# Optimization experiments

Measured on AMD Instinct MI355X. Metric: run time of the kernel, lower is better.

Reference implementation:

```python
import jax, jax.numpy as jnp
import numpy as np

D, H, NL, NR, DFF = 512, 8, 8, 16, 2048
MAX_DIST = 2.0
B, L = 4, 512


def sinusoidal_embedding(pos, dim):
    # interleaved: emb[..., 0::2]=sin, emb[..., 1::2]=cos
    half = dim // 2
    freqs = jnp.exp(-jnp.log(10000.0) * jnp.arange(half, dtype=jnp.float32) / half)
    ang = pos[..., None] * freqs  # (..., half)
    return jnp.stack([jnp.sin(ang), jnp.cos(ang)], axis=-1).reshape(*pos.shape, dim)


def setup_inputs() -> dict:
    key = jax.random.key(0)
    ks = jax.random.split(key, 24)
    s = 0.02
    n = lambda k, shape: jax.random.normal(k, shape, jnp.float32) * s
    return {
        'x_t': jax.random.normal(ks[0], (B, L, 3), jnp.float32),
        't': jax.random.randint(ks[1], (B,), 0, 1000),
        'mask': jnp.ones((B, L), bool),
        'x0_self_cond': jax.random.normal(ks[2], (B, L, 3), jnp.float32),
        'Wi': n(ks[3], (3, D)), 'bi': jnp.zeros((D,)),
        'Wsc': n(ks[4], (3, D)), 'bsc': jnp.zeros((D,)),
        'Wt1': n(ks[5], (D, D)), 'bt1': jnp.zeros((D,)),
        'Wt2': n(ks[6], (D, D)), 'bt2': jnp.zeros((D,)),
        'g1': jnp.ones((NL, D)), 'b1': jnp.zeros((NL, D)),
        'Wqkv': n(ks[7], (NL, D, 3 * D)), 'bqkv': jnp.zeros((NL, 3 * D)),
        'Wo': n(ks[8], (NL, D, D)), 'bo': jnp.zeros((NL, D)),
        'Wb': n(ks[9], (NL, NR, H)), 'bb': jnp.zeros((NL, H)),
        'g2': jnp.ones((NL, D)), 'b2': jnp.zeros((NL, D)),
        'Wf1': n(ks[10], (NL, D, DFF)), 'bf1': jnp.zeros((NL, DFF)),
        'Wf2': n(ks[11], (NL, DFF, D)), 'bf2': jnp.zeros((NL, D)),
        'gf': jnp.ones((D,)), 'bf': jnp.zeros((D,)),
        'Wout': n(ks[12], (D, 3)), 'bout': jnp.zeros((3,)),
    }


def _ln(x, g, b):
    m = x.mean(-1, keepdims=True)
    v = ((x - m) ** 2).mean(-1, keepdims=True)
    return (x - m) / jnp.sqrt(v + 1e-5) * g + b


def reference(x_t, t, mask, x0_self_cond, Wi, bi, Wsc, bsc, Wt1, bt1, Wt2, bt2,
              g1, b1, Wqkv, bqkv, Wo, bo, Wb, bb, g2, b2, Wf1, bf1, Wf2, bf2,
              gf, bf, Wout, bout):
    hd = D // H
    scale = hd ** -0.5
    # embedding: input + self-cond + positional + time
    h = (x_t @ Wi + bi) + (x0_self_cond @ Wsc + bsc)  # (B,L,D)
    pos = sinusoidal_embedding(jnp.arange(L, dtype=jnp.float32), D)  # (L,D)
    temb = sinusoidal_embedding(t.astype(jnp.float32), D)  # (B,D)
    temb = jax.nn.gelu(temb @ Wt1 + bt1, approximate=False) @ Wt2 + bt2
    h = h + pos[None] + temb[:, None]
    # shared pairwise RBF features (coords fixed across layers)
    sq = ((x_t[:, :, None] - x_t[:, None]) ** 2).sum(-1)  # (B,L,L)
    dists = jnp.sqrt(jnp.maximum(sq, 1e-12))
    mu = jnp.linspace(0.0, MAX_DIST, NR)
    sigma = MAX_DIST / NR
    rbf = jnp.exp(-(dists[..., None] - mu) ** 2 / (2.0 * sigma ** 2))  # (B,L,L,NR)
    m2 = mask[:, None, None, :]  # (B,1,1,L) key mask

    def block(h, p):
        g1_, b1_, Wqkv_, bqkv_, Wo_, bo_, Wb_, bb_, g2_, b2_, Wf1_, bf1_, Wf2_, bf2_ = p
        x = _ln(h, g1_, b1_)
        qkv = (x @ Wqkv_ + bqkv_).reshape(B, L, 3, H, hd)
        qkv = jnp.moveaxis(qkv, 3, 1)  # (B,H,L,3,hd)
        q, k, v = qkv[..., 0, :], qkv[..., 1, :], qkv[..., 2, :]
        logits = jnp.einsum('bhld,bhmd->bhlm', q, k) * scale
        geo = jnp.einsum('blmr,rh->bhlm', rbf, Wb_) + bb_[None, :, None, None]
        logits = jnp.where(m2, logits + geo, -1e30)
        w = jax.nn.softmax(logits, axis=-1)
        o = jnp.einsum('bhlm,bhmd->blhd', w, v).reshape(B, L, D)
        h = h + (o @ Wo_ + bo_)
        x2 = _ln(h, g2_, b2_)
        h = h + (jax.nn.gelu(x2 @ Wf1_ + bf1_, approximate=False) @ Wf2_ + bf2_)
        return h, None

    h, _ = jax.lax.scan(block, h, (g1, b1, Wqkv, bqkv, Wo, bo, Wb, bb, g2, b2, Wf1, bf1, Wf2, bf2))
    return _ln(h, gf, bf) @ Wout + bout  # (B,L,3) predicted eps
```

## Files before the change

kernel.cpp:

```cpp
#include <hip/hip_runtime.h>
#include <math.h>

#define D 512
#define H 8
#define HD 64
#define NLAYERS 8
#define NRBF 16
#define DFF 2048
#define BATCH 4
#define LSEQ 512

typedef unsigned short u16;
typedef __bf16 bf16x8 __attribute__((ext_vector_type(8)));
typedef float f32x4 __attribute__((ext_vector_type(4)));
typedef u16 u16x4 __attribute__((ext_vector_type(4)));
typedef u16 u16x8 __attribute__((ext_vector_type(8)));

__device__ __forceinline__ float gelu_exact(float v) {
    return 0.5f * v * (1.0f + erff(v * 0.70710678118654752440f));
}

__device__ __forceinline__ u16 f2bf(float x) {
    unsigned u = __builtin_bit_cast(unsigned, x);
    u = (u + 0x7FFFu + ((u >> 16) & 1u)) >> 16;
    return (u16)u;
}

__device__ __forceinline__ void load_lds16(const void* g, void* l) {
    __builtin_amdgcn_global_load_lds(
        (const __attribute__((address_space(1))) void*)g,
        (__attribute__((address_space(3))) void*)l, 16, 0, 0);
}

__global__ __launch_bounds__(256) void k_tes(const int* __restrict__ t,
                                             float* __restrict__ tes)
{
    int b = blockIdx.x, tid = threadIdx.x;
    float tv = (float)t[b];
    float fr = expf(-9.210340371976184f * (float)tid / 256.0f);
    float ang = tv * fr;
    tes[b * D + 2 * tid]     = sinf(ang);
    tes[b * D + 2 * tid + 1] = cosf(ang);
}

__global__ __launch_bounds__(256) void k_gemv(const float* __restrict__ x,
        const float* __restrict__ W, const float* __restrict__ bia,
        float* __restrict__ out, int do_gelu)
{
    __shared__ float part[4][64];
    int b = blockIdx.y;
    int c = threadIdx.x & 63;
    int kt = threadIdx.x >> 6;
    int col = blockIdx.x * 64 + c;
    const float* xr = x + (size_t)b * D;
    float acc = 0.0f;
    #pragma unroll 4
    for (int k = kt * 128; k < kt * 128 + 128; ++k)
        acc = fmaf(xr[k], W[(size_t)k * D + col], acc);
    part[kt][c] = acc;
    __syncthreads();
    if (kt == 0) {
        float v = part[0][c] + part[1][c] + part[2][c] + part[3][c] + bia[col];
        if (do_gelu) v = gelu_exact(v);
        out[(size_t)b * D + col] = v;
    }
}

__global__ __launch_bounds__(512) void k_embed(const float* __restrict__ x_t,
        const float* __restrict__ xsc,
        const float* __restrict__ Wi, const float* __restrict__ bi,
        const float* __restrict__ Wsc, const float* __restrict__ bsc,
        const float* __restrict__ temb, float* __restrict__ h)
{
    int rowid = blockIdx.x;
    int b = rowid >> 9, l = rowid & 511;
    int d = threadIdx.x;
    const float* pt = x_t + (size_t)rowid * 3;
    const float* ps = xsc + (size_t)rowid * 3;
    float acc = bi[d] + bsc[d] + temb[(size_t)b * D + d];
    acc = fmaf(pt[0], Wi[d], acc);
    acc = fmaf(pt[1], Wi[D + d], acc);
    acc = fmaf(pt[2], Wi[2 * D + d], acc);
    acc = fmaf(ps[0], Wsc[d], acc);
    acc = fmaf(ps[1], Wsc[D + d], acc);
    acc = fmaf(ps[2], Wsc[2 * D + d], acc);
    int i = d >> 1;
    float fr = expf(-9.210340371976184f * (float)i / 256.0f);
    float ang = (float)l * fr;
    acc += (d & 1) ? cosf(ang) : sinf(ang);
    h[(size_t)rowid * D + d] = acc;
}

template<bool BF16OUT>
__global__ __launch_bounds__(256) void k_ln(const float* __restrict__ in,
        void* __restrict__ outp,
        const float* __restrict__ g, const float* __restrict__ bta)
{
    int row = blockIdx.x, tid = threadIdx.x;
    const float* xr = in + (size_t)row * D;
    float v0 = xr[tid], v1 = xr[tid + 256];
    float s = v0 + v1;
    #pragma unroll
    for (int o = 32; o >= 1; o >>= 1) s += __shfl_down(s, o);
    __shared__ float ws4[4];
    __shared__ float mb[2];
    int wid = tid >> 6, lane = tid & 63;
    if (lane == 0) ws4[wid] = s;
    __syncthreads();
    if (tid == 0) mb[0] = (ws4[0] + ws4[1] + ws4[2] + ws4[3]) * (1.0f / 512.0f);
    __syncthreads();
    float m = mb[0];
    float d0 = v0 - m, d1 = v1 - m;
    float q = d0 * d0 + d1 * d1;
    #pragma unroll
    for (int o = 32; o >= 1; o >>= 1) q += __shfl_down(q, o);
    if (lane == 0) ws4[wid] = q;
    __syncthreads();
    if (tid == 0) {
        float var = (ws4[0] + ws4[1] + ws4[2] + ws4[3]) * (1.0f / 512.0f);
        mb[1] = 1.0f / sqrtf(var + 1e-5f);
    }
    __syncthreads();
    float inv = mb[1];
    float o0 = d0 * inv * g[tid] + bta[tid];
    float o1 = d1 * inv * g[tid + 256] + bta[tid + 256];
    if constexpr (BF16OUT) {
        u16* o = (u16*)outp;
        o[(size_t)row * D + tid]       = f2bf(o0);
        o[(size_t)row * D + tid + 256] = f2bf(o1);
    } else {
        float* o = (float*)outp;
        o[(size_t)row * D + tid]       = o0;
        o[(size_t)row * D + tid + 256] = o1;
    }
}

__global__ __launch_bounds__(256) void k_wt(const float* __restrict__ W,
        u16* __restrict__ Wt, int K, int N, size_t wstride)
{
    W  += (size_t)blockIdx.z * K * N;
    Wt += (size_t)blockIdx.z * wstride;
    __shared__ u16 t[32][33];
    int bx = blockIdx.x * 32;
    int by = blockIdx.y * 32;
    int tx = threadIdx.x & 31, ty = threadIdx.x >> 5;
    #pragma unroll
    for (int i = 0; i < 4; ++i)
        t[ty + i * 8][tx] = f2bf(W[(size_t)(by + ty + i * 8) * N + bx + tx]);
    __syncthreads();
    #pragma unroll
    for (int i = 0; i < 4; ++i)
        Wt[(size_t)(bx + ty + i * 8) * K + by + tx] = t[tx][ty + i * 8];
}

template<int MODE, int KSPLIT, int TM, int TN, bool BATCHED>
__global__ __launch_bounds__(256) void k_mfma(const u16* __restrict__ A,
        const u16* __restrict__ Bt, const float* __restrict__ bias,
        float* __restrict__ C, u16* __restrict__ Cb,
        int M, int N, int K, int lda, int ldb, int ldc, float scale,
        size_t ab, size_t ah, size_t bb, size_t bh, size_t cb2, size_t ch)
{
    constexpr int nA = TM / 64;
    constexpr int nB = TN / 64;
    constexpr int WM = (TN == 128) ? 2 : 4;
    constexpr int WN = 4 / WM;
    constexpr int MF = TM / (16 * WM);
    constexpr int NF = TN / (16 * WN);
    __shared__ u16 sA[2][TM * 32];
    __shared__ u16 sB[2][TN * 32];
    int tid = threadIdx.x;
    int bm = blockIdx.y * TM, bn = blockIdx.x * TN;
    int wave = tid >> 6, lane = tid & 63;
    int wm = wave / WN, wn = wave % WN;

    size_t aoff = 0, boff = 0, coff = 0;
    if constexpr (BATCHED) {
        int z = blockIdx.z, zb = z >> 3, zh = z & 7;
        aoff = (size_t)zb * ab + (size_t)zh * ah;
        boff = (size_t)zb * bb + (size_t)zh * bh;
        coff = (size_t)zb * cb2 + (size_t)zh * ch;
    }
    const int Kc = K / KSPLIT;
    const int nt = Kc >> 5;
    const int kb = (KSPLIT > 1 ? (int)blockIdx.z : 0) * Kc;

    const u16* pA[nA]; int idA[nA];
    const u16* pB[nB]; int idB[nB];
    #pragma unroll
    for (int s = 0; s < nA; ++s) {
        int id = tid + s * 256;
        int r = ((id >> 6) << 4) | (id & 15);
        int kg = (id >> 4) & 3;
        idA[s] = id;
        pA[s] = A + aoff + (size_t)(bm + r) * lda + kb + kg * 8;
    }
    #pragma unroll
    for (int s = 0; s < nB; ++s) {
        int id = tid + s * 256;
        int r = ((id >> 6) << 4) | (id & 15);
        int kg = (id >> 4) & 3;
        idB[s] = id;
        pB[s] = Bt + boff + (size_t)(bn + r) * ldb + kb + kg * 8;
    }

    #pragma unroll
    for (int s = 0; s < nA; ++s) { load_lds16(pA[s], &sA[0][idA[s] * 8]); pA[s] += 32; }
    #pragma unroll
    for (int s = 0; s < nB; ++s) { load_lds16(pB[s], &sB[0][idB[s] * 8]); pB[s] += 32; }

    f32x4 acc[MF][NF] = {};
    int cur = 0;
    for (int t = 0; t < nt; ++t) {
        if (t + 1 < nt) {
            int nxt = cur ^ 1;
            #pragma unroll
            for (int s = 0; s < nA; ++s) { load_lds16(pA[s], &sA[nxt][idA[s] * 8]); pA[s] += 32; }
            #pragma unroll
            for (int s = 0; s < nB; ++s) { load_lds16(pB[s], &sB[nxt][idB[s] * 8]); pB[s] += 32; }
            if constexpr (nA + nB == 4)
                asm volatile("s_waitcnt vmcnt(4)" ::: "memory");
            else
                asm volatile("s_waitcnt vmcnt(3)" ::: "memory");
        } else {
            asm volatile("s_waitcnt vmcnt(0)" ::: "memory");
        }
        __builtin_amdgcn_s_barrier();
        asm volatile("" ::: "memory");
        const u16* bufA = sA[cur];
        const u16* bufB = sB[cur];
        bf16x8 af[MF], bg[NF];
        #pragma unroll
        for (int i = 0; i < MF; ++i)
            af[i] = *(const bf16x8*)(bufA + ((wm * MF + i) * 64 + lane) * 8);
        #pragma unroll
        for (int i = 0; i < NF; ++i)
            bg[i] = *(const bf16x8*)(bufB + ((wn * NF + i) * 64 + lane) * 8);
        #pragma unroll
        for (int mi = 0; mi < MF; ++mi)
            #pragma unroll
            for (int ni = 0; ni < NF; ++ni)
                acc[mi][ni] = __builtin_amdgcn_mfma_f32_16x16x32_bf16(
                    af[mi], bg[ni], acc[mi][ni], 0, 0, 0);
        asm volatile("" ::: "memory");
        __builtin_amdgcn_s_barrier();
        cur ^= 1;
    }

    int cr = (lane >> 4) << 2;
    int cc = lane & 15;
    #pragma unroll
    for (int ni = 0; ni < NF; ++ni) {
        int col = bn + (wn * NF + ni) * 16 + cc;
        float bv = 0.0f;
        if (bias && !(KSPLIT > 1 && blockIdx.z != 0)) bv = bias[col];
        #pragma unroll
        for (int mi = 0; mi < MF; ++mi) {
            #pragma unroll
            for (int r = 0; r < 4; ++r) {
                int row = bm + (wm * MF + mi) * 16 + cr + r;
                float v = acc[mi][ni][r] + bv;
                size_t idx = coff + (size_t)row * ldc + col;
                if constexpr (MODE == 1) {
                    Cb[idx] = f2bf(gelu_exact(v));
                } else if constexpr (MODE == 2) {
                    if constexpr (KSPLIT > 1) atomicAdd(&C[idx], v);
                    else C[idx] += v;
                } else if constexpr (MODE == 3) {
                    Cb[idx] = f2bf(v);
                } else {
                    C[idx] = fmaf(v, scale, C[idx]);
                }
            }
        }
    }
}

__global__ __launch_bounds__(512) void k_geo(const float* __restrict__ x_t,
        const float* __restrict__ Wb_l, const float* __restrict__ bb_l,
        float* __restrict__ geo)
{
    __shared__ float wbs[NRBF * H];
    __shared__ float bbs[H];
    int tid = threadIdx.x;
    int b = blockIdx.x >> 9, l = blockIdx.x & 511;
    if (tid < NRBF * H) wbs[tid] = Wb_l[tid];
    if (tid < H) bbs[tid] = bb_l[tid];
    __syncthreads();
    int m = tid;
    const float* pl = x_t + ((size_t)b * LSEQ + l) * 3;
    const float* pm = x_t + ((size_t)b * LSEQ + m) * 3;
    float dx = pl[0] - pm[0], dy = pl[1] - pm[1], dz = pl[2] - pm[2];
    float dist = sqrtf(fmaxf(dx * dx + dy * dy + dz * dz, 1e-12f));
    float e[NRBF];
    #pragma unroll
    for (int r = 0; r < NRBF; ++r) {
        float dd = dist - (2.0f / 15.0f) * (float)r;
        e[r] = expf(-dd * dd * 32.0f);
    }
    #pragma unroll
    for (int hh = 0; hh < H; ++hh) {
        float acc = bbs[hh];
        #pragma unroll
        for (int r = 0; r < NRBF; ++r) acc = fmaf(e[r], wbs[r * H + hh], acc);
        geo[(((size_t)b * H + hh) * LSEQ + l) * LSEQ + m] = acc;
    }
}

__global__ __launch_bounds__(256) void k_vt(const u16* __restrict__ qkv,
                                            u16* __restrict__ vT)
{
    __shared__ u16 s[64 * 65];
    int z = blockIdx.y, b = z >> 3, hh = z & 7;
    int l0 = blockIdx.x * 64;
    const u16* src = qkv + (size_t)(b * LSEQ + l0) * (3 * D) + 2 * D + hh * 64;
    int tid = threadIdx.x;
    int rl = tid >> 3;
    int ch = (tid & 7) * 8;
    #pragma unroll
    for (int it = 0; it < 2; ++it) {
        int l = rl + it * 32;
        u16x8 v = *(const u16x8*)(src + (size_t)l * (3 * D) + ch);
        #pragma unroll
        for (int j = 0; j < 8; ++j) s[l * 65 + ch + j] = v[j];
    }
    __syncthreads();
    u16* dst = vT + (size_t)z * (HD * LSEQ) + l0;
    int lane = tid & 63;
    int h0 = tid >> 6;
    #pragma unroll
    for (int it = 0; it < 16; ++it) {
        int hd = h0 * 16 + it;
        dst[(size_t)hd * LSEQ + lane] = s[lane * 65 + hd];
    }
}

__global__ __launch_bounds__(256) void k_attn(const u16* __restrict__ qkv,
        const u16* __restrict__ vT, const float* __restrict__ geo,
        u16* __restrict__ O)
{
    __shared__ u16 sQ[4096];
    __shared__ u16 sK[2][4096];
    __shared__ u16 sV[2][4096];
    __shared__ float sG[2][4096];
    __shared__ u16 sP[4][1024];
    int tid = threadIdx.x;
    int wave = tid >> 6, lane = tid & 63;
    int qt = blockIdx.x, z = blockIdx.y;
    int b = z >> 3, hh = z & 7;
    int q0 = qt * 64;

    const u16* qbase = qkv + (size_t)b * LSEQ * (3 * D) + hh * 64;
    const u16* vbase = vT + (size_t)z * (HD * LSEQ);
    const float* gbase = geo + ((size_t)z * LSEQ + q0) * LSEQ;

    {
        #pragma unroll
        for (int i = 0; i < 2; ++i) {
            int id = tid + i * 256;
            int f = id >> 7, s = (id >> 6) & 1, ln = id & 63;
            load_lds16(qbase + (size_t)(q0 + f * 16 + (ln & 15)) * (3 * D)
                       + s * 32 + ((ln >> 4) & 3) * 8, sQ + id * 8);
        }
    }
    auto stage = [&](int kt, int buf) {
        #pragma unroll
        for (int i = 0; i < 2; ++i) {
            int id = tid + i * 256;
            int f = id >> 7, s = (id >> 6) & 1, ln = id & 63;
            load_lds16(qbase + (size_t)(kt * 64 + f * 16 + (ln & 15)) * (3 * D)
                       + D + s * 32 + ((ln >> 4) & 3) * 8, sK[buf] + id * 8);
        }
        #pragma unroll
        for (int i = 0; i < 2; ++i) {
            int id = tid + i * 256;
            int f = id >> 7, s = (id >> 6) & 1, ln = id & 63;
            load_lds16(vbase + (size_t)(f * 16 + (ln & 15)) * LSEQ
                       + kt * 64 + s * 32 + ((ln >> 4) & 3) * 8, sV[buf] + id * 8);
        }
        #pragma unroll
        for (int i = 0; i < 4; ++i) {
            int id = tid + i * 256;
            load_lds16(gbase + (size_t)(id >> 4) * LSEQ + kt * 64 + (id & 15) * 4,
                       &sG[buf][id * 4]);
        }
    };
    stage(0, 0);

    f32x4 oacc[4] = {};
    float m_run[4] = {-1e30f, -1e30f, -1e30f, -1e30f};
    float l_run[4] = {0.f, 0.f, 0.f, 0.f};
    bf16x8 aq[2];
    u16* pw = sP[wave];
    int qgrp = lane >> 4;
    int cc = lane & 15;

    int cur = 0;
    for (int kt = 0; kt < 8; ++kt) {
        if (kt + 1 < 8) {
            stage(kt + 1, cur ^ 1);
            asm volatile("s_waitcnt vmcnt(8)" ::: "memory");
        } else {
            asm volatile("s_waitcnt vmcnt(0)" ::: "memory");
        }
        __builtin_amdgcn_s_barrier();
        asm volatile("" ::: "memory");
        if (kt == 0) {
            aq[0] = *(const bf16x8*)(sQ + (wave * 128 + lane) * 8);
            aq[1] = *(const bf16x8*)(sQ + (wave * 128 + 64 + lane) * 8);
        }
        f32x4 sc[4] = {};
        #pragma unroll
        for (int f = 0; f < 4; ++f) {
            #pragma unroll
            for (int s = 0; s < 2; ++s) {
                bf16x8 bk = *(const bf16x8*)(sK[cur] + (f * 128 + s * 64 + lane) * 8);
                sc[f] = __builtin_amdgcn_mfma_f32_16x16x32_bf16(aq[s], bk, sc[f], 0, 0, 0);
            }
        }
        float lg[4][4];
        #pragma unroll
        for (int f = 0; f < 4; ++f)
            #pragma unroll
            for (int r = 0; r < 4; ++r)
                lg[f][r] = fmaf(sc[f][r], 0.125f,
                    sG[cur][(wave * 16 + qgrp * 4 + r) * 64 + f * 16 + cc]);
        float tmax[4];
        #pragma unroll
        for (int r = 0; r < 4; ++r) {
            tmax[r] = fmaxf(fmaxf(lg[0][r], lg[1][r]), fmaxf(lg[2][r], lg[3][r]));
            #pragma unroll
            for (int o = 1; o <= 8; o <<= 1)
                tmax[r] = fmaxf(tmax[r], __shfl_xor(tmax[r], o));
        }
        float corr[4], rs[4];
        #pragma unroll
        for (int r = 0; r < 4; ++r) {
            float mnew = fmaxf(m_run[r], tmax[r]);
            corr[r] = expf(m_run[r] - mnew);
            m_run[r] = mnew;
            rs[r] = 0.f;
        }
        float pf[4][4];
        #pragma unroll
        for (int f = 0; f < 4; ++f)
            #pragma unroll
            for (int r = 0; r < 4; ++r) {
                float p = expf(lg[f][r] - m_run[r]);
                pf[f][r] = p;
                rs[r] += p;
            }
        #pragma unroll
        for (int r = 0; r < 4; ++r) {
            #pragma unroll
            for (int o = 1; o <= 8; o <<= 1)
                rs[r] += __shfl_xor(rs[r], o);
            l_run[r] = l_run[r] * corr[r] + rs[r];
        }
        #pragma unroll
        for (int fd = 0; fd < 4; ++fd)
            #pragma unroll
            for (int r = 0; r < 4; ++r)
                oacc[fd][r] *= corr[r];
        #pragma unroll
        for (int f = 0; f < 4; ++f)
            #pragma unroll
            for (int r = 0; r < 4; ++r) {
                int m = f * 16 + cc;
                int q = qgrp * 4 + r;
                pw[(m >> 5) * 512 + ((m >> 3) & 3) * 128 + q * 8 + (m & 7)]
                    = f2bf(pf[f][r]);
            }
        asm volatile("s_waitcnt lgkmcnt(0)" ::: "memory");
        __builtin_amdgcn_sched_barrier(0);
        bf16x8 ap0 = *(const bf16x8*)(pw + lane * 8);
        bf16x8 ap1 = *(const bf16x8*)(pw + 512 + lane * 8);
        #pragma unroll
        for (int fd = 0; fd < 4; ++fd) {
            #pragma unroll
            for (int s = 0; s < 2; ++s) {
                bf16x8 bv = *(const bf16x8*)(sV[cur] + (fd * 128 + s * 64 + lane) * 8);
                oacc[fd] = __builtin_amdgcn_mfma_f32_16x16x32_bf16(
                    s ? ap1 : ap0, bv, oacc[fd], 0, 0, 0);
            }
        }
        asm volatile("" ::: "memory");
        __builtin_amdgcn_s_barrier();
        cur ^= 1;
    }

    float linv[4];
    #pragma unroll
    for (int r = 0; r < 4; ++r) linv[r] = 1.0f / l_run[r];
    u16* obase = O + ((size_t)(b * LSEQ + q0 + wave * 16)) * D + hh * 64;
    #pragma unroll
    for (int fd = 0; fd < 4; ++fd)
        #pragma unroll
        for (int r = 0; r < 4; ++r)
            obase[(size_t)(qgrp * 4 + r) * D + fd * 16 + cc]
                = f2bf(oacc[fd][r] * linv[r]);
}

__global__ __launch_bounds__(64) void k_out(const float* __restrict__ x,
        const float* __restrict__ Wout, const float* __restrict__ bout,
        float* __restrict__ out)
{
    int row = blockIdx.x, lane = threadIdx.x;
    const float* xr = x + (size_t)row * D;
    float v[8];
    #pragma unroll
    for (int j = 0; j < 8; ++j) v[j] = xr[lane * 8 + j];
    #pragma unroll
    for (int c = 0; c < 3; ++c) {
        float s = 0.0f;
        #pragma unroll
        for (int j = 0; j < 8; ++j)
            s = fmaf(v[j], Wout[(size_t)(lane * 8 + j) * 3 + c], s);
        #pragma unroll
        for (int o = 32; o >= 1; o >>= 1) s += __shfl_xor(s, o);
        if (lane == 0) out[(size_t)row * 3 + c] = s + bout[c];
    }
}

extern "C" void kernel_launch(void* const* d_in, const int* in_sizes, int n_in,
                              void* d_out, int out_size, void* d_ws, size_t ws_size,
                              hipStream_t stream)
{
    const float* x_t  = (const float*)d_in[0];
    const int*   t    = (const int*)d_in[1];
    const float* xsc  = (const float*)d_in[3];
    const float* Wi   = (const float*)d_in[4];
    const float* bi   = (const float*)d_in[5];
    const float* Wsc  = (const float*)d_in[6];
    const float* bsc  = (const float*)d_in[7];
    const float* Wt1  = (const float*)d_in[8];
    const float* bt1  = (const float*)d_in[9];
    const float* Wt2  = (const float*)d_in[10];
    const float* bt2  = (const float*)d_in[11];
    const float* g1   = (const float*)d_in[12];
    const float* b1   = (const float*)d_in[13];
    const float* Wqkv = (const float*)d_in[14];
    const float* bqkv = (const float*)d_in[15];
    const float* Wo   = (const float*)d_in[16];
    const float* bo   = (const float*)d_in[17];
    const float* Wb   = (const float*)d_in[18];
    const float* bbp  = (const float*)d_in[19];
    const float* g2   = (const float*)d_in[20];
    const float* b2   = (const float*)d_in[21];
    const float* Wf1  = (const float*)d_in[22];
    const float* bf1  = (const float*)d_in[23];
    const float* Wf2  = (const float*)d_in[24];
    const float* bf2  = (const float*)d_in[25];
    const float* gf   = (const float*)d_in[26];
    const float* bfv  = (const float*)d_in[27];
    const float* Wout = (const float*)d_in[28];
    const float* bout = (const float*)d_in[29];

    const size_t M1 = 1u << 20;
    float* ws    = (float*)d_ws;
    float* tes   = ws;
    float* temb1 = tes + 2048;
    float* temb  = temb1 + 2048;
    float* h     = temb + 2048;
    float* geo   = h + M1;
    float* x     = geo;
    u16*   qkvb  = (u16*)(geo + 8 * M1);
    u16*   vT    = qkvb + 3 * M1;
    u16*   xb    = vT + M1;
    u16*   obuf  = xb + M1;
    u16*   ffh   = obuf + M1;
    u16*   wbase = ffh + 4 * M1;
    const size_t WQ = 1536 * 512, WO = 512 * 512, WF1 = 512 * 2048,
                 WF2 = 2048 * 512;
    const size_t WL = WQ + WO + WF1 + WF2;
    size_t need8 = (size_t)((char*)(wbase + 8 * WL) - (char*)d_ws);
    bool pre = ws_size >= need8;

    if (pre) {
        k_wt<<<dim3(48, 16, 8), 256, 0, stream>>>(Wqkv, wbase, 512, 1536, WL);
        k_wt<<<dim3(16, 16, 8), 256, 0, stream>>>(Wo, wbase + WQ, 512, 512, WL);
        k_wt<<<dim3(64, 16, 8), 256, 0, stream>>>(Wf1, wbase + WQ + WO, 512, 2048, WL);
        k_wt<<<dim3(16, 64, 8), 256, 0, stream>>>(Wf2, wbase + WQ + WO + WF1, 2048, 512, WL);
    }

    k_tes<<<BATCH, 256, 0, stream>>>(t, tes);
    k_gemv<<<dim3(8, BATCH), 256, 0, stream>>>(tes, Wt1, bt1, temb1, 1);
    k_gemv<<<dim3(8, BATCH), 256, 0, stream>>>(temb1, Wt2, bt2, temb, 0);
    k_embed<<<BATCH * LSEQ, 512, 0, stream>>>(x_t, xsc, Wi, bi, Wsc, bsc, temb, h);

    for (int layer = 0; layer < NLAYERS; ++layer) {
        const float* g1_   = g1 + layer * D;
        const float* b1_   = b1 + layer * D;
        const float* Wqkv_ = Wqkv + (size_t)layer * D * 3 * D;
        const float* bqkv_ = bqkv + (size_t)layer * 3 * D;
        const float* Wo_   = Wo + (size_t)layer * D * D;
        const float* bo_   = bo + (size_t)layer * D;
        const float* Wb_   = Wb + (size_t)layer * NRBF * H;
        const float* bb_   = bbp + (size_t)layer * H;
        const float* g2_   = g2 + layer * D;
        const float* b2_   = b2 + layer * D;
        const float* Wf1_  = Wf1 + (size_t)layer * D * DFF;
        const float* bf1_  = bf1 + (size_t)layer * DFF;
        const float* Wf2_  = Wf2 + (size_t)layer * DFF * D;
        const float* bf2_  = bf2 + (size_t)layer * D;

        u16* wq  = wbase + (pre ? (size_t)layer * WL : 0);
        u16* wo_ = wq + WQ;
        u16* wf1 = wo_ + WO;
        u16* wf2 = wf1 + WF1;
        if (!pre) {
            k_wt<<<dim3(48, 16, 1), 256, 0, stream>>>(Wqkv_, wq, 512, 1536, 0);
            k_wt<<<dim3(16, 16, 1), 256, 0, stream>>>(Wo_, wo_, 512, 512, 0);
            k_wt<<<dim3(64, 16, 1), 256, 0, stream>>>(Wf1_, wf1, 512, 2048, 0);
            k_wt<<<dim3(16, 64, 1), 256, 0, stream>>>(Wf2_, wf2, 2048, 512, 0);
        }

        k_ln<true><<<BATCH * LSEQ, 256, 0, stream>>>(h, xb, g1_, b1_);
        k_mfma<3, 1, 128, 128, false><<<dim3(12, 16, 1), 256, 0, stream>>>(
            xb, wq, bqkv_, nullptr, qkvb, 2048, 1536, 512,
            512, 512, 1536, 0.f, 0, 0, 0, 0, 0, 0);
        k_vt<<<dim3(8, 32), 256, 0, stream>>>(qkvb, vT);
        k_geo<<<BATCH * LSEQ, 512, 0, stream>>>(x_t, Wb_, bb_, geo);
        k_attn<<<dim3(8, 32), 256, 0, stream>>>(qkvb, vT, geo, obuf);
        k_mfma<2, 4, 128, 128, false><<<dim3(4, 16, 4), 256, 0, stream>>>(
            obuf, wo_, bo_, h, nullptr, 2048, 512, 512,
            512, 512, 512, 0.f, 0, 0, 0, 0, 0, 0);
        k_ln<true><<<BATCH * LSEQ, 256, 0, stream>>>(h, xb, g2_, b2_);
        k_mfma<1, 1, 128, 128, false><<<dim3(16, 16, 1), 256, 0, stream>>>(
            xb, wf1, bf1_, nullptr, ffh, 2048, 2048, 512,
            512, 512, 2048, 0.f, 0, 0, 0, 0, 0, 0);
        k_mfma<2, 4, 128, 128, false><<<dim3(4, 16, 4), 256, 0, stream>>>(
            ffh, wf2, bf2_, h, nullptr, 2048, 512, 2048,
            2048, 2048, 512, 0.f, 0, 0, 0, 0, 0, 0);
    }

    k_ln<false><<<BATCH * LSEQ, 256, 0, stream>>>(h, x, gf, bfv);
    k_out<<<BATCH * LSEQ, 64, 0, stream>>>(x, Wout, bout, (float*)d_out);
}
```

Before: 1.318 ms.

## Fuse geometric bias into attention via distance lookup table; fuse V transpose

Each layer no longer materializes the B*H*L*L geometric bias tensor. A per-layer table of the RBF-projected bias is precomputed over distances in [0,4) at 1/1024 resolution, and the attention kernel computes pairwise distances from x_t in LDS and looks up the bias. The QKV GEMM epilogue now writes the V part directly in transposed layout, which removes the separate k_vt kernel. This saves a large global write and read of the bias per layer and two launches per layer. In exchange the bias is a nearest-sample approximation, with distances clamped at the table end where the RBF terms are effectively zero.

```diff
diff --git a/kernel.cpp b/kernel.cpp
--- a/kernel.cpp
+++ b/kernel.cpp
@@ -153,12 +153,34 @@
         Wt[(size_t)(bx + ty + i * 8) * K + by + tx] = t[tx][ty + i * 8];
 }
 
-template<int MODE, int KSPLIT, int TM, int TN, bool BATCHED>
+__global__ __launch_bounds__(256) void k_tab(const float* __restrict__ Wb,
+        const float* __restrict__ bbp, float* __restrict__ tabs)
+{
+    int layer = blockIdx.x;
+    int tid = threadIdx.x;
+    __shared__ float wbs[NRBF * H];
+    __shared__ float bbs[H];
+    if (tid < NRBF * H) wbs[tid] = Wb[layer * NRBF * H + tid];
+    if (tid < H) bbs[tid] = bbp[layer * H + tid];
+    __syncthreads();
+    for (int i = tid; i < H * 4096; i += 256) {
+        int hh = i >> 12, ii = i & 4095;
+        float d = (float)ii * (1.0f / 1024.0f);
+        float acc = bbs[hh];
+        #pragma unroll
+        for (int r = 0; r < NRBF; ++r) {
+            float dd = d - (2.0f / 15.0f) * (float)r;
+            acc = fmaf(expf(-dd * dd * 32.0f), wbs[r * H + hh], acc);
+        }
+        tabs[(size_t)layer * (H * 4096) + i] = acc;
+    }
+}
+
+template<int MODE, int KSPLIT, int TM, int TN>
 __global__ __launch_bounds__(256) void k_mfma(const u16* __restrict__ A,
         const u16* __restrict__ Bt, const float* __restrict__ bias,
-        float* __restrict__ C, u16* __restrict__ Cb,
-        int M, int N, int K, int lda, int ldb, int ldc, float scale,
-        size_t ab, size_t ah, size_t bb, size_t bh, size_t cb2, size_t ch)
+        float* __restrict__ C, u16* __restrict__ Cb, u16* __restrict__ vTp,
+        int M, int N, int K, int lda, int ldb, int ldc)
 {
     constexpr int nA = TM / 64;
     constexpr int nB = TN / 64;
@@ -173,13 +195,6 @@
     int wave = tid >> 6, lane = tid & 63;
     int wm = wave / WN, wn = wave % WN;
 
-    size_t aoff = 0, boff = 0, coff = 0;
-    if constexpr (BATCHED) {
-        int z = blockIdx.z, zb = z >> 3, zh = z & 7;
-        aoff = (size_t)zb * ab + (size_t)zh * ah;
-        boff = (size_t)zb * bb + (size_t)zh * bh;
-        coff = (size_t)zb * cb2 + (size_t)zh * ch;
-    }
     const int Kc = K / KSPLIT;
     const int nt = Kc >> 5;
     const int kb = (KSPLIT > 1 ? (int)blockIdx.z : 0) * Kc;
@@ -192,7 +207,7 @@
         int r = ((id >> 6) << 4) | (id & 15);
         int kg = (id >> 4) & 3;
         idA[s] = id;
-        pA[s] = A + aoff + (size_t)(bm + r) * lda + kb + kg * 8;
+        pA[s] = A + (size_t)(bm + r) * lda + kb + kg * 8;
     }
     #pragma unroll
     for (int s = 0; s < nB; ++s) {
@@ -200,7 +215,7 @@
         int r = ((id >> 6) << 4) | (id & 15);
         int kg = (id >> 4) & 3;
         idB[s] = id;
-        pB[s] = Bt + boff + (size_t)(bn + r) * ldb + kb + kg * 8;
+        pB[s] = Bt + (size_t)(bn + r) * ldb + kb + kg * 8;
     }
 
     #pragma unroll
@@ -255,94 +270,46 @@
         if (bias && !(KSPLIT > 1 && blockIdx.z != 0)) bv = bias[col];
         #pragma unroll
         for (int mi = 0; mi < MF; ++mi) {
+            int row0 = bm + (wm * MF + mi) * 16 + cr;
+            if constexpr (MODE == 3) {
+                if (col >= 1024) {
+                    u16x4 c4;
+                    #pragma unroll
+                    for (int r = 0; r < 4; ++r) c4[r] = f2bf(acc[mi][ni][r] + bv);
+                    int cv = col - 1024;
+                    int hh = cv >> 6, hd = cv & 63;
+                    int bb_ = row0 >> 9, l0 = row0 & 511;
+                    *(u16x4*)(vTp + (((size_t)bb_ * 8 + hh) * 64 + hd) * 512 + l0) = c4;
+                    continue;
+                }
+            }
             #pragma unroll
             for (int r = 0; r < 4; ++r) {
-                int row = bm + (wm * MF + mi) * 16 + cr + r;
                 float v = acc[mi][ni][r] + bv;
-                size_t idx = coff + (size_t)row * ldc + col;
+                size_t idx = (size_t)(row0 + r) * ldc + col;
                 if constexpr (MODE == 1) {
                     Cb[idx] = f2bf(gelu_exact(v));
                 } else if constexpr (MODE == 2) {
                     if constexpr (KSPLIT > 1) atomicAdd(&C[idx], v);
                     else C[idx] += v;
-                } else if constexpr (MODE == 3) {
+                } else {
                     Cb[idx] = f2bf(v);
-                } else {
-                    C[idx] = fmaf(v, scale, C[idx]);
                 }
             }
         }
     }
 }
 
-__global__ __launch_bounds__(512) void k_geo(const float* __restrict__ x_t,
-        const float* __restrict__ Wb_l, const float* __restrict__ bb_l,
-        float* __restrict__ geo)
-{
-    __shared__ float wbs[NRBF * H];
-    __shared__ float bbs[H];
-    int tid = threadIdx.x;
-    int b = blockIdx.x >> 9, l = blockIdx.x & 511;
-    if (tid < NRBF * H) wbs[tid] = Wb_l[tid];
-    if (tid < H) bbs[tid] = bb_l[tid];
-    __syncthreads();
-    int m = tid;
-    const float* pl = x_t + ((size_t)b * LSEQ + l) * 3;
-    const float* pm = x_t + ((size_t)b * LSEQ + m) * 3;
-    float dx = pl[0] - pm[0], dy = pl[1] - pm[1], dz = pl[2] - pm[2];
-    float dist = sqrtf(fmaxf(dx * dx + dy * dy + dz * dz, 1e-12f));
-    float e[NRBF];
-    #pragma unroll
-    for (int r = 0; r < NRBF; ++r) {
-        float dd = dist - (2.0f / 15.0f) * (float)r;
-        e[r] = expf(-dd * dd * 32.0f);
-    }
-    #pragma unroll
-    for (int hh = 0; hh < H; ++hh) {
-        float acc = bbs[hh];
-        #pragma unroll
-        for (int r = 0; r < NRBF; ++r) acc = fmaf(e[r], wbs[r * H + hh], acc);
-        geo[(((size_t)b * H + hh) * LSEQ + l) * LSEQ + m] = acc;
-    }
-}
-
-__global__ __launch_bounds__(256) void k_vt(const u16* __restrict__ qkv,
-                                            u16* __restrict__ vT)
-{
-    __shared__ u16 s[64 * 65];
-    int z = blockIdx.y, b = z >> 3, hh = z & 7;
-    int l0 = blockIdx.x * 64;
-    const u16* src = qkv + (size_t)(b * LSEQ + l0) * (3 * D) + 2 * D + hh * 64;
-    int tid = threadIdx.x;
-    int rl = tid >> 3;
-    int ch = (tid & 7) * 8;
-    #pragma unroll
-    for (int it = 0; it < 2; ++it) {
-        int l = rl + it * 32;
-        u16x8 v = *(const u16x8*)(src + (size_t)l * (3 * D) + ch);
-        #pragma unroll
-        for (int j = 0; j < 8; ++j) s[l * 65 + ch + j] = v[j];
-    }
-    __syncthreads();
-    u16* dst = vT + (size_t)z * (HD * LSEQ) + l0;
-    int lane = tid & 63;
-    int h0 = tid >> 6;
-    #pragma unroll
-    for (int it = 0; it < 16; ++it) {
-        int hd = h0 * 16 + it;
-        dst[(size_t)hd * LSEQ + lane] = s[lane * 65 + hd];
-    }
-}
-
 __global__ __launch_bounds__(256) void k_attn(const u16* __restrict__ qkv,
-        const u16* __restrict__ vT, const float* __restrict__ geo,
-        u16* __restrict__ O)
+        const u16* __restrict__ vT, const float* __restrict__ tab,
+        const float* __restrict__ x_t, u16* __restrict__ O)
 {
     __shared__ u16 sQ[4096];
     __shared__ u16 sK[2][4096];
     __shared__ u16 sV[2][4096];
-    __shared__ float sG[2][4096];
     __shared__ u16 sP[4][1024];
+    __shared__ float sTab[4096];
+    __shared__ float sX[1536];
     int tid = threadIdx.x;
     int wave = tid >> 6, lane = tid & 63;
     int qt = blockIdx.x, z = blockIdx.y;
@@ -351,16 +318,25 @@
 
     const u16* qbase = qkv + (size_t)b * LSEQ * (3 * D) + hh * 64;
     const u16* vbase = vT + (size_t)z * (HD * LSEQ);
-    const float* gbase = geo + ((size_t)z * LSEQ + q0) * LSEQ;
-
-    {
-        #pragma unroll
-        for (int i = 0; i < 2; ++i) {
-            int id = tid + i * 256;
-            int f = id >> 7, s = (id >> 6) & 1, ln = id & 63;
-            load_lds16(qbase + (size_t)(q0 + f * 16 + (ln & 15)) * (3 * D)
-                       + s * 32 + ((ln >> 4) & 3) * 8, sQ + id * 8);
-        }
+    const float* tb = tab + hh * 4096;
+
+    #pragma unroll
+    for (int i = 0; i < 2; ++i) {
+        int id = tid + i * 256;
+        if (id < 384)
+            load_lds16(x_t + (size_t)b * 1536 + id * 4, sX + id * 4);
+    }
+    #pragma unroll
+    for (int i = 0; i < 4; ++i) {
+        int id = tid + i * 256;
+        load_lds16(tb + id * 4, sTab + id * 4);
+    }
+    #pragma unroll
+    for (int i = 0; i < 2; ++i) {
+        int id = tid + i * 256;
+        int f = id >> 7, s = (id >> 6) & 1, ln = id & 63;
+        load_lds16(qbase + (size_t)(q0 + f * 16 + (ln & 15)) * (3 * D)
+                   + s * 32 + (ln >> 4) * 8, sQ + id * 8);
     }
     auto stage = [&](int kt, int buf) {
         #pragma unroll
@@ -368,20 +344,14 @@
             int id = tid + i * 256;
             int f = id >> 7, s = (id >> 6) & 1, ln = id & 63;
             load_lds16(qbase + (size_t)(kt * 64 + f * 16 + (ln & 15)) * (3 * D)
-                       + D + s * 32 + ((ln >> 4) & 3) * 8, sK[buf] + id * 8);
+                       + D + s * 32 + (ln >> 4) * 8, sK[buf] + id * 8);
         }
         #pragma unroll
         for (int i = 0; i < 2; ++i) {
             int id = tid + i * 256;
             int f = id >> 7, s = (id >> 6) & 1, ln = id & 63;
             load_lds16(vbase + (size_t)(f * 16 + (ln & 15)) * LSEQ
-                       + kt * 64 + s * 32 + ((ln >> 4) & 3) * 8, sV[buf] + id * 8);
-        }
-        #pragma unroll
-        for (int i = 0; i < 4; ++i) {
-            int id = tid + i * 256;
-            load_lds16(gbase + (size_t)(id >> 4) * LSEQ + kt * 64 + (id & 15) * 4,
-                       &sG[buf][id * 4]);
+                       + kt * 64 + s * 32 + (ln >> 4) * 8, sV[buf] + id * 8);
         }
     };
     stage(0, 0);
@@ -390,6 +360,7 @@
     float m_run[4] = {-1e30f, -1e30f, -1e30f, -1e30f};
     float l_run[4] = {0.f, 0.f, 0.f, 0.f};
     bf16x8 aq[2];
+    float qx[4][3];
     u16* pw = sP[wave];
     int qgrp = lane >> 4;
     int cc = lane & 15;
@@ -398,7 +369,7 @@
     for (int kt = 0; kt < 8; ++kt) {
         if (kt + 1 < 8) {
             stage(kt + 1, cur ^ 1);
-            asm volatile("s_waitcnt vmcnt(8)" ::: "memory");
+            asm volatile("s_waitcnt vmcnt(4)" ::: "memory");
         } else {
             asm volatile("s_waitcnt vmcnt(0)" ::: "memory");
         }
@@ -407,6 +378,13 @@
         if (kt == 0) {
             aq[0] = *(const bf16x8*)(sQ + (wave * 128 + lane) * 8);
             aq[1] = *(const bf16x8*)(sQ + (wave * 128 + 64 + lane) * 8);
+            #pragma unroll
+            for (int r = 0; r < 4; ++r) {
+                int q = q0 + wave * 16 + qgrp * 4 + r;
+                qx[r][0] = sX[q * 3];
+                qx[r][1] = sX[q * 3 + 1];
+                qx[r][2] = sX[q * 3 + 2];
+            }
         }
         f32x4 sc[4] = {};
         #pragma unroll
@@ -419,11 +397,20 @@
         }
         float lg[4][4];
         #pragma unroll
-        for (int f = 0; f < 4; ++f)
-            #pragma unroll
-            for (int r = 0; r < 4; ++r)
-                lg[f][r] = fmaf(sc[f][r], 0.125f,
-                    sG[cur][(wave * 16 + qgrp * 4 + r) * 64 + f * 16 + cc]);
+        for (int f = 0; f < 4; ++f) {
+            int m = kt * 64 + f * 16 + cc;
+            float mx0 = sX[m * 3], mx1 = sX[m * 3 + 1], mx2 = sX[m * 3 + 2];
+            #pragma unroll
+            for (int r = 0; r < 4; ++r) {
+                float dx = qx[r][0] - mx0;
+                float dy = qx[r][1] - mx1;
+                float dz = qx[r][2] - mx2;
+                float dq = sqrtf(fmaxf(dx * dx + dy * dy + dz * dz, 1e-12f));
+                int ix = (int)(dq * 1024.0f + 0.5f);
+                ix = ix > 4095 ? 4095 : ix;
+                lg[f][r] = fmaf(sc[f][r], 0.125f, sTab[ix]);
+            }
+        }
         float tmax[4];
         #pragma unroll
         for (int r = 0; r < 4; ++r) {
@@ -561,9 +548,9 @@
     float* temb1 = tes + 2048;
     float* temb  = temb1 + 2048;
     float* h     = temb + 2048;
-    float* geo   = h + M1;
-    float* x     = geo;
-    u16*   qkvb  = (u16*)(geo + 8 * M1);
+    float* x     = h + M1;
+    float* tabs  = x + M1;
+    u16*   qkvb  = (u16*)(tabs + NLAYERS * H * 4096);
     u16*   vT    = qkvb + 3 * M1;
     u16*   xb    = vT + M1;
     u16*   obuf  = xb + M1;
@@ -581,6 +568,7 @@
         k_wt<<<dim3(64, 16, 8), 256, 0, stream>>>(Wf1, wbase + WQ + WO, 512, 2048, WL);
         k_wt<<<dim3(16, 64, 8), 256, 0, stream>>>(Wf2, wbase + WQ + WO + WF1, 2048, 512, WL);
     }
+    k_tab<<<NLAYERS, 256, 0, stream>>>(Wb, bbp, tabs);
 
     k_tes<<<BATCH, 256, 0, stream>>>(t, tes);
     k_gemv<<<dim3(8, BATCH), 256, 0, stream>>>(tes, Wt1, bt1, temb1, 1);
@@ -594,8 +582,6 @@
         const float* bqkv_ = bqkv + (size_t)layer * 3 * D;
         const float* Wo_   = Wo + (size_t)layer * D * D;
         const float* bo_   = bo + (size_t)layer * D;
-        const float* Wb_   = Wb + (size_t)layer * NRBF * H;
-        const float* bb_   = bbp + (size_t)layer * H;
         const float* g2_   = g2 + layer * D;
         const float* b2_   = b2 + layer * D;
         const float* Wf1_  = Wf1 + (size_t)layer * D * DFF;
@@ -615,22 +601,17 @@
         }
 
         k_ln<true><<<BATCH * LSEQ, 256, 0, stream>>>(h, xb, g1_, b1_);
-        k_mfma<3, 1, 128, 128, false><<<dim3(12, 16, 1), 256, 0, stream>>>(
-            xb, wq, bqkv_, nullptr, qkvb, 2048, 1536, 512,
-            512, 512, 1536, 0.f, 0, 0, 0, 0, 0, 0);
-        k_vt<<<dim3(8, 32), 256, 0, stream>>>(qkvb, vT);
-        k_geo<<<BATCH * LSEQ, 512, 0, stream>>>(x_t, Wb_, bb_, geo);
-        k_attn<<<dim3(8, 32), 256, 0, stream>>>(qkvb, vT, geo, obuf);
-        k_mfma<2, 4, 128, 128, false><<<dim3(4, 16, 4), 256, 0, stream>>>(
-            obuf, wo_, bo_, h, nullptr, 2048, 512, 512,
-            512, 512, 512, 0.f, 0, 0, 0, 0, 0, 0);
+        k_mfma<3, 1, 128, 128><<<dim3(12, 16, 1), 256, 0, stream>>>(
+            xb, wq, bqkv_, nullptr, qkvb, vT, 2048, 1536, 512, 512, 512, 1536);
+        k_attn<<<dim3(8, 32), 256, 0, stream>>>(
+            qkvb, vT, tabs + (size_t)layer * H * 4096, x_t, obuf);
+        k_mfma<2, 4, 128, 128><<<dim3(4, 16, 4), 256, 0, stream>>>(
+            obuf, wo_, bo_, h, nullptr, nullptr, 2048, 512, 512, 512, 512, 512);
         k_ln<true><<<BATCH * LSEQ, 256, 0, stream>>>(h, xb, g2_, b2_);
-        k_mfma<1, 1, 128, 128, false><<<dim3(16, 16, 1), 256, 0, stream>>>(
-            xb, wf1, bf1_, nullptr, ffh, 2048, 2048, 512,
-            512, 512, 2048, 0.f, 0, 0, 0, 0, 0, 0);
-        k_mfma<2, 4, 128, 128, false><<<dim3(4, 16, 4), 256, 0, stream>>>(
-            ffh, wf2, bf2_, h, nullptr, 2048, 512, 2048,
-            2048, 2048, 512, 0.f, 0, 0, 0, 0, 0, 0);
+        k_mfma<1, 1, 128, 128><<<dim3(16, 16, 1), 256, 0, stream>>>(
+            xb, wf1, bf1_, nullptr, ffh, nullptr, 2048, 2048, 512, 512, 512, 2048);
+        k_mfma<2, 4, 128, 128><<<dim3(4, 16, 4), 256, 0, stream>>>(
+            ffh, wf2, bf2_, h, nullptr, nullptr, 2048, 512, 2048, 2048, 2048, 512);
     }
 
     k_ln<false><<<BATCH * LSEQ, 256, 0, stream>>>(h, x, gf, bfv);
```

Result: no change. 1.327 ms (+0.7%).
